# Performance work log

Measured on AMD Instinct MI355X. Metric: run time of the kernel, lower is better.

The kernel has to match this reference:

```python
import jax, jax.numpy as jnp
import numpy as np

FS = 11        # filter_size
N_ITER = 5     # mean-field iterations


def _unfold(x, fs):
    """x: (B, C, Hp, Wp) padded -> patches (B, C, H, W, fs, fs) with
    patches[b,c,h,w,i,j] == x[b,c,h+i,w+j]."""
    B, C, Hp, Wp = x.shape
    H, W = Hp - fs + 1, Wp - fs + 1
    p = jax.lax.conv_general_dilated_patches(
        x.reshape(B * C, 1, Hp, Wp), (fs, fs), (1, 1), 'VALID')  # (B*C, fs*fs, H, W)
    return p.reshape(B, C, fs, fs, H, W).transpose(0, 1, 4, 5, 2, 3)


def _smoothing_filter(fs, inv_bw, spacings):
    """Gaussian spatial filter with zeroed center, shape (B, fs, fs)."""
    r = jnp.arange(-(fs // 2), fs // 2 + 1, dtype=spacings.dtype)
    d = jnp.stack(jnp.meshgrid(r, r, indexing='ij'))           # (2, fs, fs)
    d = d[None] * spacings[:, :, None, None]                   # (B, 2, fs, fs)
    f = jnp.exp(-jnp.sum((d * inv_bw) ** 2 / 2, axis=1))       # (B, fs, fs)
    return f.at[:, fs // 2, fs // 2].set(0.0)


def setup_inputs() -> dict:
    key = jax.random.key(0)
    k1, k2 = jax.random.split(key)
    B, C, CH, H, W = 2, 6, 3, 192, 192
    return {
        'x': jax.random.normal(k1, (B, C, H, W), dtype=jnp.float32),
        'features': jax.random.normal(k2, (B, CH, H, W), dtype=jnp.float32),
        'spatial_spacings': jnp.ones((B, 2), dtype=jnp.float32),
        'smoothing_weight': jnp.array(1.0, dtype=jnp.float32),
        'appearance_weight': jnp.array(1.0, dtype=jnp.float32),
        'inverse_smoothing_bandwidth': jnp.array(1.0, dtype=jnp.float32),
        'inverse_appearance_bandwidth': jnp.array(1.0, dtype=jnp.float32),
    }


def reference(x, features, spatial_spacings, smoothing_weight, appearance_weight,
              inverse_smoothing_bandwidth, inverse_appearance_bandwidth):
    fs, pad = FS, FS // 2
    B, C, H, W = x.shape
    pad_cfg = [(0, 0), (0, 0), (pad, pad), (pad, pad)]

    # Spatial Gaussian filter (iteration-independent).
    sf = _smoothing_filter(fs, inverse_smoothing_bandwidth, spatial_spacings)  # (B,fs,fs)

    # Bilateral (appearance) filter, also iteration-independent -> hoisted.
    fpatch = _unfold(jnp.pad(features, pad_cfg), fs)           # (B,ch,H,W,fs,fs)
    diffs = features[..., None, None] - fpatch
    af = jnp.exp(-jnp.sum((diffs * inverse_appearance_bandwidth) ** 2 / 2, axis=1))  # (B,H,W,fs,fs)
    af = af.at[..., fs // 2, fs // 2].set(0.0)

    # combined message filter: w_s * sf + w_a * sf * af  (center tap already zero)
    sfb = sf[:, None, None]                                    # (B,1,1,fs,fs)
    total_filter = smoothing_weight * jnp.broadcast_to(sfb, af.shape) + appearance_weight * sfb * af

    compat = -jnp.eye(C, dtype=x.dtype)                        # Potts compatibility mu(l,l') = -[l==l']
    negative_unary = x
    for _ in range(N_ITER):
        q = jax.nn.softmax(x, axis=1)
        qpatch = _unfold(jnp.pad(q, pad_cfg), fs)              # (B,C,H,W,fs,fs)
        msg = jnp.einsum('bhwij,bchwij->bchw', total_filter, qpatch)
        x = negative_unary - jnp.einsum('bjhw,jk->bkhw', msg, compat)
    return jax.nn.log_softmax(x, axis=1)
```

## Files before the change

kernel.cpp:

```cpp
#include <hip/hip_runtime.h>

#define HH 192
#define WW 192
#define BB 2
#define NC 6
#define FSZ 11
#define PAD 5
#define TW 16
#define TH 8
#define SWD 26
#define SHT 18
#define LA 33
#define HW (HH*WW)
#define BT 512

__device__ __forceinline__ unsigned pkbf(float a, float b) {
    unsigned ua = (__float_as_uint(a) + 0x8000u) >> 16;
    unsigned ub = (__float_as_uint(b) + 0x8000u) & 0xffff0000u;
    return ua | ub;
}
__device__ __forceinline__ float lo16(unsigned u){ return __uint_as_float(u << 16); }
__device__ __forceinline__ float hi16(unsigned u){ return __uint_as_float(u & 0xffff0000u); }

template<bool FIRST, bool LAST>
__global__ __launch_bounds__(BT, 4)
void crf_iter(const float* __restrict__ xpl, const uint4* __restrict__ Ain,
              const float* __restrict__ f2in, const float* __restrict__ feats,
              const float* __restrict__ spac, const float* __restrict__ swp,
              const float* __restrict__ awp, const float* __restrict__ isbp,
              const float* __restrict__ iabp,
              uint4* __restrict__ Aout, float* __restrict__ f2out,
              float* __restrict__ outp)
{
    __shared__ uint4 A[SHT][LA];
    __shared__ float F2[SHT][LA];
    __shared__ float sfw[FSZ*FSZ];
    __shared__ float sfa[FSZ*FSZ];
    __shared__ float pm[8][NC][132];

    const int tid = threadIdx.x;
    const int b  = blockIdx.z;
    const int w0 = blockIdx.x * TW;
    const int h0 = blockIdx.y * TH;

    const float swv = swp[0], awv = awp[0], isb = isbp[0], iab = iabp[0];
    const float s0 = spac[b*2], s1 = spac[b*2+1];
    const float sfac = iab * 0.70710678f;

    if (tid < FSZ*FSZ) {
        const int fi = tid / FSZ, fj = tid - (tid/FSZ)*FSZ;
        const float ri = (float)(fi-PAD) * s0 * isb;
        const float rj = (float)(fj-PAD) * s1 * isb;
        float sf = __expf(-0.5f*(ri*ri + rj*rj));
        if (fi == PAD && fj == PAD) sf = 0.f;
        sfw[tid] = sf * swv;
        sfa[tid] = sf * awv;
    }

    for (int idx = tid; idx < SHT*SWD; idx += BT) {
        const int sr = idx / SWD, sc = idx - (idx/SWD)*SWD;
        const int gh = h0 + sr - PAD, gw = w0 + sc - PAD;
        uint4 av = make_uint4(0u,0u,0u,0u);
        float f2v = 0.f;
        if (gh >= 0 && gh < HH && gw >= 0 && gw < WW) {
            if (FIRST) {
                const int off = gh*WW + gw;
                const float* xb = xpl + (size_t)b*NC*HW + off;
                const float v0 = xb[0];
                const float v1 = xb[HW];
                const float v2 = xb[2*HW];
                const float v3 = xb[3*HW];
                const float v4 = xb[4*HW];
                const float v5 = xb[5*HW];
                float m = fmaxf(fmaxf(fmaxf(v0,v1),fmaxf(v2,v3)),fmaxf(v4,v5));
                float q0=__expf(v0-m), q1=__expf(v1-m), q2=__expf(v2-m);
                float q3=__expf(v3-m), q4=__expf(v4-m), q5=__expf(v5-m);
                const float rs = 1.0f/(q0+q1+q2+q3+q4+q5);
                q0*=rs; q1*=rs; q2*=rs; q3*=rs; q4*=rs; q5*=rs;
                const float* fb = feats + (size_t)b*3*HW + off;
                const float g0 = fb[0]*sfac, g1 = fb[HW]*sfac, g2 = fb[2*HW]*sfac;
                av = make_uint4(pkbf(q0,q1), pkbf(q2,q3), pkbf(q4,q5), pkbf(g0,g1));
                f2v = g2;
            } else {
                const size_t p = (size_t)(b*HH + gh)*WW + gw;
                av  = Ain[p];
                f2v = f2in[p];
            }
        }
        A[sr][sc]  = av;
        F2[sr][sc] = f2v;
    }

    const int w    = tid >> 6;
    const int l    = tid & 63;
    const int half = l >> 5;
    const int lh   = l & 31;
    const int ry   = lh >> 2;
    const int lc0  = (lh & 3) * 4;
    const int jb   = half * 6;

    __syncthreads();

    float cf0[4], cf1[4], cf2[4];
    #pragma unroll
    for (int k = 0; k < 4; ++k) {
        const unsigned fw = A[ry+PAD][lc0+PAD+k].w;
        cf0[k] = lo16(fw);
        cf1[k] = hi16(fw);
        cf2[k] = F2[ry+PAD][lc0+PAD+k];
    }

    float msg[4][NC];
    #pragma unroll
    for (int k = 0; k < 4; ++k)
        #pragma unroll
        for (int c = 0; c < NC; ++c) msg[k][c] = 0.f;

    auto row_pass = [&](int i) {
        const int r = ry + i;
        const uint4* Ar = &A[r][lc0 + jb];
        const float* Fr = &F2[r][lc0 + jb];
        float srwR[6], sraR[6];
        #pragma unroll
        for (int d = 0; d < 6; ++d) {
            const int jj = jb + d;
            const bool v = (jj < FSZ);
            srwR[d] = v ? sfw[i*FSZ + jj] : 0.f;
            sraR[d] = v ? sfa[i*FSZ + jj] : 0.f;
        }
        #pragma unroll
        for (int a = 0; a < 8; ++a) {
            const uint4 av = Ar[a];
            const float g2 = Fr[a];
            const float q0 = lo16(av.x), q1 = hi16(av.x);
            const float q2 = lo16(av.y), q3 = hi16(av.y);
            const float q4 = lo16(av.z), q5 = hi16(av.z);
            const float g0 = lo16(av.w), g1 = hi16(av.w);
            #pragma unroll
            for (int k = 0; k < 4; ++k) {
                const int d = a - k;
                if (d < 0 || d > 5) continue;
                const float d0 = cf0[k]-g0, d1 = cf1[k]-g1, d2 = cf2[k]-g2;
                const float t  = fmaf(d2,d2, fmaf(d1,d1, d0*d0));
                const float af = __expf(-t);
                const float tf = fmaf(af, sraR[d], srwR[d]);
                msg[k][0] = fmaf(tf,q0,msg[k][0]);
                msg[k][1] = fmaf(tf,q1,msg[k][1]);
                msg[k][2] = fmaf(tf,q2,msg[k][2]);
                msg[k][3] = fmaf(tf,q3,msg[k][3]);
                msg[k][4] = fmaf(tf,q4,msg[k][4]);
                msg[k][5] = fmaf(tf,q5,msg[k][5]);
            }
        }
        if (jb == 0) {
            const uint4 av = Ar[8];
            const float g2 = Fr[8];
            const float q0 = lo16(av.x), q1 = hi16(av.x);
            const float q2 = lo16(av.y), q3 = hi16(av.y);
            const float q4 = lo16(av.z), q5 = hi16(av.z);
            const float g0 = lo16(av.w), g1 = hi16(av.w);
            const float d0 = cf0[3]-g0, d1 = cf1[3]-g1, d2 = cf2[3]-g2;
            const float t  = fmaf(d2,d2, fmaf(d1,d1, d0*d0));
            const float af = __expf(-t);
            const float tf = fmaf(af, sraR[5], srwR[5]);
            msg[3][0] = fmaf(tf,q0,msg[3][0]);
            msg[3][1] = fmaf(tf,q1,msg[3][1]);
            msg[3][2] = fmaf(tf,q2,msg[3][2]);
            msg[3][3] = fmaf(tf,q3,msg[3][3]);
            msg[3][4] = fmaf(tf,q4,msg[3][4]);
            msg[3][5] = fmaf(tf,q5,msg[3][5]);
        }
    };

    row_pass(w);
    if (w < 3) row_pass(w + 8);

    #pragma unroll
    for (int k = 0; k < 4; ++k)
        #pragma unroll
        for (int c = 0; c < NC; ++c)
            msg[k][c] += __shfl_xor(msg[k][c], 32);

    if (half == 0) {
        #pragma unroll
        for (int c = 0; c < NC; ++c) {
            float4 v = make_float4(msg[0][c], msg[1][c], msg[2][c], msg[3][c]);
            *(float4*)&pm[w][c][ry*16 + lc0] = v;
        }
    }
    __syncthreads();

    if (tid < TW*TH) {
        const int col = tid & 15, rw = tid >> 4;
        float xn[NC];
        #pragma unroll
        for (int c = 0; c < NC; ++c) {
            float s = 0.f;
            #pragma unroll
            for (int g = 0; g < 8; ++g) s += pm[g][c][tid];
            xn[c] = s;
        }
        const int gh = h0 + rw, gw = w0 + col;
        const size_t pb = (size_t)b*NC*HW + (size_t)gh*WW + gw;
        #pragma unroll
        for (int c = 0; c < NC; ++c) xn[c] += xpl[pb + (size_t)c*HW];

        float m = xn[0];
        #pragma unroll
        for (int c = 1; c < NC; ++c) m = fmaxf(m, xn[c]);

        if (LAST) {
            float s = 0.f;
            #pragma unroll
            for (int c = 0; c < NC; ++c) s += __expf(xn[c]-m);
            const float lg = m + __logf(s);
            #pragma unroll
            for (int c = 0; c < NC; ++c) outp[pb + (size_t)c*HW] = xn[c] - lg;
        } else {
            float e[NC]; float s = 0.f;
            #pragma unroll
            for (int c = 0; c < NC; ++c) { e[c] = __expf(xn[c]-m); s += e[c]; }
            const float rs = 1.0f / s;
            const unsigned f01 = A[rw+PAD][col+PAD].w;
            const size_t p = (size_t)(b*HH + gh)*WW + gw;
            Aout[p] = make_uint4(pkbf(e[0]*rs, e[1]*rs),
                                 pkbf(e[2]*rs, e[3]*rs),
                                 pkbf(e[4]*rs, e[5]*rs), f01);
            if (FIRST) f2out[p] = F2[rw+PAD][col+PAD];
        }
    }
}

extern "C" void kernel_launch(void* const* d_in, const int* in_sizes, int n_in,
                              void* d_out, int out_size, void* d_ws, size_t ws_size,
                              hipStream_t stream)
{
    const float* x    = (const float*)d_in[0];
    const float* fts  = (const float*)d_in[1];
    const float* spc  = (const float*)d_in[2];
    const float* swp  = (const float*)d_in[3];
    const float* awp  = (const float*)d_in[4];
    const float* isbp = (const float*)d_in[5];
    const float* iabp = (const float*)d_in[6];
    float* out = (float*)d_out;

    uint4* A0  = (uint4*)d_ws;
    uint4* A1  = A0 + (size_t)BB*HW;
    float* f2s = (float*)(A1 + (size_t)BB*HW);

    dim3 grid(WW/TW, HH/TH, BB);
    dim3 blk(BT);

    crf_iter<true ,false><<<grid, blk, 0, stream>>>(x, A1, f2s, fts, spc, swp, awp, isbp, iabp, A0, f2s, out);
    crf_iter<false,false><<<grid, blk, 0, stream>>>(x, A0, f2s, fts, spc, swp, awp, isbp, iabp, A1, f2s, out);
    crf_iter<false,false><<<grid, blk, 0, stream>>>(x, A1, f2s, fts, spc, swp, awp, isbp, iabp, A0, f2s, out);
    crf_iter<false,false><<<grid, blk, 0, stream>>>(x, A0, f2s, fts, spc, swp, awp, isbp, iabp, A1, f2s, out);
    crf_iter<false,true ><<<grid, blk, 0, stream>>>(x, A1, f2s, fts, spc, swp, awp, isbp, iabp, A0, f2s, out);
}
```

Measured before the change: 64.34 us.

## Fuse two mean-field iterations per kernel using halo recomputation

Each launch now runs two CRF iterations. The first iteration is computed over an expanded tile that includes the filter halo, and its softmax result is kept in shared memory as the input to the second iteration. The final iteration runs in a separate kernel that applies log-softmax, so the launch count drops from five to three and the intermediate global round-trips are reduced. In exchange, the first stage of each pair recomputes messages for the whole halo region, which greatly increases exp and FMA work per output pixel. Thread utilisation also changes: 234 of 512 lanes-pairs are used in the first stage, and the second stage uses a 4-way row split.

```diff
diff --git a/kernel.cpp b/kernel.cpp
--- a/kernel.cpp
+++ b/kernel.cpp
@@ -8,11 +8,15 @@
 #define PAD 5
 #define TW 16
 #define TH 8
-#define SWD 26
-#define SHT 18
-#define LA 33
+#define SW2 36
+#define SH2 28
+#define LA1 37
+#define MW 26
+#define MH 18
+#define LA2 27
 #define HW (HH*WW)
 #define BT 512
+#define NPAIR 234
 
 __device__ __forceinline__ unsigned pkbf(float a, float b) {
     unsigned ua = (__float_as_uint(a) + 0x8000u) >> 16;
@@ -22,31 +26,9 @@
 __device__ __forceinline__ float lo16(unsigned u){ return __uint_as_float(u << 16); }
 __device__ __forceinline__ float hi16(unsigned u){ return __uint_as_float(u & 0xffff0000u); }
 
-template<bool FIRST, bool LAST>
-__global__ __launch_bounds__(BT, 4)
-void crf_iter(const float* __restrict__ xpl, const uint4* __restrict__ Ain,
-              const float* __restrict__ f2in, const float* __restrict__ feats,
-              const float* __restrict__ spac, const float* __restrict__ swp,
-              const float* __restrict__ awp, const float* __restrict__ isbp,
-              const float* __restrict__ iabp,
-              uint4* __restrict__ Aout, float* __restrict__ f2out,
-              float* __restrict__ outp)
+__device__ __forceinline__ void build_sf(int tid, float s0, float s1, float isb,
+                                         float swv, float awv, float* sfw, float* sfa)
 {
-    __shared__ uint4 A[SHT][LA];
-    __shared__ float F2[SHT][LA];
-    __shared__ float sfw[FSZ*FSZ];
-    __shared__ float sfa[FSZ*FSZ];
-    __shared__ float pm[8][NC][132];
-
-    const int tid = threadIdx.x;
-    const int b  = blockIdx.z;
-    const int w0 = blockIdx.x * TW;
-    const int h0 = blockIdx.y * TH;
-
-    const float swv = swp[0], awv = awp[0], isb = isbp[0], iab = iabp[0];
-    const float s0 = spac[b*2], s1 = spac[b*2+1];
-    const float sfac = iab * 0.70710678f;
-
     if (tid < FSZ*FSZ) {
         const int fi = tid / FSZ, fj = tid - (tid/FSZ)*FSZ;
         const float ri = (float)(fi-PAD) * s0 * isb;
@@ -56,30 +38,53 @@
         sfw[tid] = sf * swv;
         sfa[tid] = sf * awv;
     }
-
-    for (int idx = tid; idx < SHT*SWD; idx += BT) {
-        const int sr = idx / SWD, sc = idx - (idx/SWD)*SWD;
-        const int gh = h0 + sr - PAD, gw = w0 + sc - PAD;
+}
+
+template<bool FIRST>
+__global__ __launch_bounds__(BT, 4)
+void crf_pair(const float* __restrict__ xpl, const uint4* __restrict__ Ain,
+              const float* __restrict__ f2in, const float* __restrict__ feats,
+              const float* __restrict__ spac, const float* __restrict__ swp,
+              const float* __restrict__ awp, const float* __restrict__ isbp,
+              const float* __restrict__ iabp,
+              uint4* __restrict__ Aout, float* __restrict__ f2out)
+{
+    __shared__ uint4 A1[SH2][LA1];
+    __shared__ float F2a[SH2][LA1];
+    __shared__ uint4 Q1[MH][LA2];
+    __shared__ float sfw[FSZ*FSZ], sfa[FSZ*FSZ];
+    __shared__ float pm[4][NC][132];
+
+    const int tid = threadIdx.x;
+    const int b  = blockIdx.z;
+    const int w0 = blockIdx.x * TW;
+    const int h0 = blockIdx.y * TH;
+
+    const float swv = swp[0], awv = awp[0], isb = isbp[0], iab = iabp[0];
+    const float s0 = spac[b*2], s1 = spac[b*2+1];
+    const float sfac = iab * 0.70710678f;
+
+    build_sf(tid, s0, s1, isb, swv, awv, sfw, sfa);
+
+    for (int idx = tid; idx < SH2*LA1; idx += BT) {
+        const int sr = idx / LA1, sc = idx - (idx/LA1)*LA1;
+        const int gh = h0 - 2*PAD + sr, gw = w0 - 2*PAD + sc;
         uint4 av = make_uint4(0u,0u,0u,0u);
         float f2v = 0.f;
         if (gh >= 0 && gh < HH && gw >= 0 && gw < WW) {
             if (FIRST) {
                 const int off = gh*WW + gw;
                 const float* xb = xpl + (size_t)b*NC*HW + off;
-                const float v0 = xb[0];
-                const float v1 = xb[HW];
-                const float v2 = xb[2*HW];
-                const float v3 = xb[3*HW];
-                const float v4 = xb[4*HW];
-                const float v5 = xb[5*HW];
+                const float v0 = xb[0], v1 = xb[HW], v2 = xb[2*HW];
+                const float v3 = xb[3*HW], v4 = xb[4*HW], v5 = xb[5*HW];
                 float m = fmaxf(fmaxf(fmaxf(v0,v1),fmaxf(v2,v3)),fmaxf(v4,v5));
                 float q0=__expf(v0-m), q1=__expf(v1-m), q2=__expf(v2-m);
                 float q3=__expf(v3-m), q4=__expf(v4-m), q5=__expf(v5-m);
                 const float rs = 1.0f/(q0+q1+q2+q3+q4+q5);
-                q0*=rs; q1*=rs; q2*=rs; q3*=rs; q4*=rs; q5*=rs;
                 const float* fb = feats + (size_t)b*3*HW + off;
                 const float g0 = fb[0]*sfac, g1 = fb[HW]*sfac, g2 = fb[2*HW]*sfac;
-                av = make_uint4(pkbf(q0,q1), pkbf(q2,q3), pkbf(q4,q5), pkbf(g0,g1));
+                av = make_uint4(pkbf(q0*rs,q1*rs), pkbf(q2*rs,q3*rs),
+                                pkbf(q4*rs,q5*rs), pkbf(g0,g1));
                 f2v = g2;
             } else {
                 const size_t p = (size_t)(b*HH + gh)*WW + gw;
@@ -87,147 +92,264 @@
                 f2v = f2in[p];
             }
         }
-        A[sr][sc]  = av;
-        F2[sr][sc] = f2v;
-    }
-
-    const int w    = tid >> 6;
-    const int l    = tid & 63;
-    const int half = l >> 5;
-    const int lh   = l & 31;
-    const int ry   = lh >> 2;
-    const int lc0  = (lh & 3) * 4;
-    const int jb   = half * 6;
-
-    __syncthreads();
-
-    float cf0[4], cf1[4], cf2[4];
-    #pragma unroll
-    for (int k = 0; k < 4; ++k) {
-        const unsigned fw = A[ry+PAD][lc0+PAD+k].w;
-        cf0[k] = lo16(fw);
-        cf1[k] = hi16(fw);
-        cf2[k] = F2[ry+PAD][lc0+PAD+k];
-    }
-
-    float msg[4][NC];
-    #pragma unroll
-    for (int k = 0; k < 4; ++k)
-        #pragma unroll
-        for (int c = 0; c < NC; ++c) msg[k][c] = 0.f;
-
-    auto row_pass = [&](int i) {
-        const int r = ry + i;
-        const uint4* Ar = &A[r][lc0 + jb];
-        const float* Fr = &F2[r][lc0 + jb];
-        float srwR[6], sraR[6];
-        #pragma unroll
-        for (int d = 0; d < 6; ++d) {
-            const int jj = jb + d;
-            const bool v = (jj < FSZ);
-            srwR[d] = v ? sfw[i*FSZ + jj] : 0.f;
-            sraR[d] = v ? sfa[i*FSZ + jj] : 0.f;
-        }
-        #pragma unroll
-        for (int a = 0; a < 8; ++a) {
-            const uint4 av = Ar[a];
-            const float g2 = Fr[a];
-            const float q0 = lo16(av.x), q1 = hi16(av.x);
-            const float q2 = lo16(av.y), q3 = hi16(av.y);
-            const float q4 = lo16(av.z), q5 = hi16(av.z);
-            const float g0 = lo16(av.w), g1 = hi16(av.w);
+        A1[sr][sc]  = av;
+        F2a[sr][sc] = f2v;
+    }
+    __syncthreads();
+
+    {
+        const int half = tid & 1;
+        const int pr   = tid >> 1;
+        if (pr < NPAIR) {
+            const int r1 = pr / 13;
+            const int c0 = (pr - r1*13) * 2;
+            const int jb = half * 6;
+
+            const unsigned cwA = A1[r1+PAD][c0+PAD].w;
+            const unsigned cwB = A1[r1+PAD][c0+PAD+1].w;
+            const float a0 = lo16(cwA), a1 = hi16(cwA), a2 = F2a[r1+PAD][c0+PAD];
+            const float b0 = lo16(cwB), b1 = hi16(cwB), b2 = F2a[r1+PAD][c0+PAD+1];
+
+            float mA[NC], mB[NC];
             #pragma unroll
-            for (int k = 0; k < 4; ++k) {
-                const int d = a - k;
-                if (d < 0 || d > 5) continue;
-                const float d0 = cf0[k]-g0, d1 = cf1[k]-g1, d2 = cf2[k]-g2;
-                const float t  = fmaf(d2,d2, fmaf(d1,d1, d0*d0));
-                const float af = __expf(-t);
-                const float tf = fmaf(af, sraR[d], srwR[d]);
-                msg[k][0] = fmaf(tf,q0,msg[k][0]);
-                msg[k][1] = fmaf(tf,q1,msg[k][1]);
-                msg[k][2] = fmaf(tf,q2,msg[k][2]);
-                msg[k][3] = fmaf(tf,q3,msg[k][3]);
-                msg[k][4] = fmaf(tf,q4,msg[k][4]);
-                msg[k][5] = fmaf(tf,q5,msg[k][5]);
-            }
-        }
-        if (jb == 0) {
-            const uint4 av = Ar[8];
-            const float g2 = Fr[8];
-            const float q0 = lo16(av.x), q1 = hi16(av.x);
-            const float q2 = lo16(av.y), q3 = hi16(av.y);
-            const float q4 = lo16(av.z), q5 = hi16(av.z);
-            const float g0 = lo16(av.w), g1 = hi16(av.w);
-            const float d0 = cf0[3]-g0, d1 = cf1[3]-g1, d2 = cf2[3]-g2;
-            const float t  = fmaf(d2,d2, fmaf(d1,d1, d0*d0));
-            const float af = __expf(-t);
-            const float tf = fmaf(af, sraR[5], srwR[5]);
-            msg[3][0] = fmaf(tf,q0,msg[3][0]);
-            msg[3][1] = fmaf(tf,q1,msg[3][1]);
-            msg[3][2] = fmaf(tf,q2,msg[3][2]);
-            msg[3][3] = fmaf(tf,q3,msg[3][3]);
-            msg[3][4] = fmaf(tf,q4,msg[3][4]);
-            msg[3][5] = fmaf(tf,q5,msg[3][5]);
-        }
-    };
-
-    row_pass(w);
-    if (w < 3) row_pass(w + 8);
-
-    #pragma unroll
-    for (int k = 0; k < 4; ++k)
+            for (int c = 0; c < NC; ++c) { mA[c]=0.f; mB[c]=0.f; }
+
+            #pragma unroll 1
+            for (int i = 0; i < FSZ; ++i) {
+                float srwR[6], sraR[6];
+                #pragma unroll
+                for (int d = 0; d < 6; ++d) {
+                    const int jj = jb + d;
+                    const bool v = (jj < FSZ);
+                    srwR[d] = v ? sfw[i*FSZ + jj] : 0.f;
+                    sraR[d] = v ? sfa[i*FSZ + jj] : 0.f;
+                }
+                const uint4* Ar = &A1[r1+i][c0+jb];
+                const float* Fr = &F2a[r1+i][c0+jb];
+                #pragma unroll
+                for (int a = 0; a < 7; ++a) {
+                    const uint4 av = Ar[a];
+                    const float g2 = Fr[a];
+                    const float q0 = lo16(av.x), q1 = hi16(av.x);
+                    const float q2 = lo16(av.y), q3 = hi16(av.y);
+                    const float q4 = lo16(av.z), q5 = hi16(av.z);
+                    const float g0 = lo16(av.w), g1 = hi16(av.w);
+                    if (a < 6) {
+                        const float d0=a0-g0, d1=a1-g1, d2=a2-g2;
+                        const float tt = fmaf(d2,d2, fmaf(d1,d1, d0*d0));
+                        const float af = __expf(-tt);
+                        const float tf = fmaf(af, sraR[a], srwR[a]);
+                        mA[0]=fmaf(tf,q0,mA[0]); mA[1]=fmaf(tf,q1,mA[1]);
+                        mA[2]=fmaf(tf,q2,mA[2]); mA[3]=fmaf(tf,q3,mA[3]);
+                        mA[4]=fmaf(tf,q4,mA[4]); mA[5]=fmaf(tf,q5,mA[5]);
+                    }
+                    if (a >= 1) {
+                        const float d0=b0-g0, d1=b1-g1, d2=b2-g2;
+                        const float tt = fmaf(d2,d2, fmaf(d1,d1, d0*d0));
+                        const float af = __expf(-tt);
+                        const float tf = fmaf(af, sraR[a-1], srwR[a-1]);
+                        mB[0]=fmaf(tf,q0,mB[0]); mB[1]=fmaf(tf,q1,mB[1]);
+                        mB[2]=fmaf(tf,q2,mB[2]); mB[3]=fmaf(tf,q3,mB[3]);
+                        mB[4]=fmaf(tf,q4,mB[4]); mB[5]=fmaf(tf,q5,mB[5]);
+                    }
+                }
+            }
+
+            #pragma unroll
+            for (int c = 0; c < NC; ++c) {
+                mA[c] += __shfl_xor(mA[c], 1);
+                mB[c] += __shfl_xor(mB[c], 1);
+            }
+
+            if (half == 0) {
+                const int gh = h0 - PAD + r1;
+                #pragma unroll
+                for (int k = 0; k < 2; ++k) {
+                    const int gw = w0 - PAD + c0 + k;
+                    const float* msg = k ? mB : mA;
+                    uint4 qv = make_uint4(0u,0u,0u,0u);
+                    if (gh >= 0 && gh < HH && gw >= 0 && gw < WW) {
+                        const float* up = xpl + (size_t)b*NC*HW + (size_t)gh*WW + gw;
+                        float xn[NC];
+                        #pragma unroll
+                        for (int c = 0; c < NC; ++c) xn[c] = up[(size_t)c*HW] + msg[c];
+                        float m = xn[0];
+                        #pragma unroll
+                        for (int c = 1; c < NC; ++c) m = fmaxf(m, xn[c]);
+                        float e[NC], s = 0.f;
+                        #pragma unroll
+                        for (int c = 0; c < NC; ++c) { e[c] = __expf(xn[c]-m); s += e[c]; }
+                        const float rs = 1.0f / s;
+                        qv = make_uint4(pkbf(e[0]*rs,e[1]*rs), pkbf(e[2]*rs,e[3]*rs),
+                                        pkbf(e[4]*rs,e[5]*rs), k ? cwB : cwA);
+                    }
+                    Q1[r1][c0+k] = qv;
+                }
+            }
+        }
+    }
+    __syncthreads();
+
+    {
+        const int g = tid >> 7, p = tid & 127;
+        const int pr = p >> 4, pc = p & 15;
+        const unsigned cw = A1[pr+2*PAD][pc+2*PAD].w;
+        const float c0f = lo16(cw), c1f = hi16(cw), c2f = F2a[pr+2*PAD][pc+2*PAD];
+        float m2[NC];
+        #pragma unroll
+        for (int c = 0; c < NC; ++c) m2[c] = 0.f;
+
+        #pragma unroll 1
+        for (int ii = 0; ii < 3; ++ii) {
+            const int i = g + 4*ii;
+            if (i < FSZ) {
+                const float* srw = &sfw[i*FSZ];
+                const float* sra = &sfa[i*FSZ];
+                const uint4* Qr = &Q1[pr+i][pc];
+                const float* Fr = &F2a[pr+i+PAD][pc+PAD];
+                #pragma unroll
+                for (int j = 0; j < FSZ; ++j) {
+                    const uint4 av = Qr[j];
+                    const float g2 = Fr[j];
+                    const float q0 = lo16(av.x), q1 = hi16(av.x);
+                    const float q2 = lo16(av.y), q3 = hi16(av.y);
+                    const float q4 = lo16(av.z), q5 = hi16(av.z);
+                    const float g0 = lo16(av.w), g1 = hi16(av.w);
+                    const float d0=c0f-g0, d1=c1f-g1, d2=c2f-g2;
+                    const float tt = fmaf(d2,d2, fmaf(d1,d1, d0*d0));
+                    const float af = __expf(-tt);
+                    const float tf = fmaf(af, sra[j], srw[j]);
+                    m2[0]=fmaf(tf,q0,m2[0]); m2[1]=fmaf(tf,q1,m2[1]);
+                    m2[2]=fmaf(tf,q2,m2[2]); m2[3]=fmaf(tf,q3,m2[3]);
+                    m2[4]=fmaf(tf,q4,m2[4]); m2[5]=fmaf(tf,q5,m2[5]);
+                }
+            }
+        }
+        #pragma unroll
+        for (int c = 0; c < NC; ++c) pm[g][c][p] = m2[c];
+    }
+    __syncthreads();
+
+    if (tid < 128) {
+        const int pr = tid >> 4, pc = tid & 15;
+        float xn[NC];
         #pragma unroll
         for (int c = 0; c < NC; ++c)
-            msg[k][c] += __shfl_xor(msg[k][c], 32);
-
-    if (half == 0) {
-        #pragma unroll
-        for (int c = 0; c < NC; ++c) {
-            float4 v = make_float4(msg[0][c], msg[1][c], msg[2][c], msg[3][c]);
-            *(float4*)&pm[w][c][ry*16 + lc0] = v;
-        }
-    }
-    __syncthreads();
-
-    if (tid < TW*TH) {
-        const int col = tid & 15, rw = tid >> 4;
+            xn[c] = pm[0][c][tid] + pm[1][c][tid] + pm[2][c][tid] + pm[3][c][tid];
+        const int gh = h0 + pr, gw = w0 + pc;
+        const float* up = xpl + (size_t)b*NC*HW + (size_t)gh*WW + gw;
+        #pragma unroll
+        for (int c = 0; c < NC; ++c) xn[c] += up[(size_t)c*HW];
+        float m = xn[0];
+        #pragma unroll
+        for (int c = 1; c < NC; ++c) m = fmaxf(m, xn[c]);
+        float e[NC], s = 0.f;
+        #pragma unroll
+        for (int c = 0; c < NC; ++c) { e[c] = __expf(xn[c]-m); s += e[c]; }
+        const float rs = 1.0f / s;
+        const size_t p = (size_t)(b*HH + gh)*WW + gw;
+        Aout[p] = make_uint4(pkbf(e[0]*rs,e[1]*rs), pkbf(e[2]*rs,e[3]*rs),
+                             pkbf(e[4]*rs,e[5]*rs), A1[pr+2*PAD][pc+2*PAD].w);
+        if (FIRST) f2out[p] = F2a[pr+2*PAD][pc+2*PAD];
+    }
+}
+
+__global__ __launch_bounds__(BT, 4)
+void crf_last(const float* __restrict__ xpl, const uint4* __restrict__ Ain,
+              const float* __restrict__ f2in,
+              const float* __restrict__ spac, const float* __restrict__ swp,
+              const float* __restrict__ awp, const float* __restrict__ isbp,
+              const float* __restrict__ iabp, float* __restrict__ outp)
+{
+    __shared__ uint4 Ac[MH][LA2];
+    __shared__ float F2c[MH][LA2];
+    __shared__ float sfw[FSZ*FSZ], sfa[FSZ*FSZ];
+    __shared__ float pm[4][NC][132];
+
+    const int tid = threadIdx.x;
+    const int b  = blockIdx.z;
+    const int w0 = blockIdx.x * TW;
+    const int h0 = blockIdx.y * TH;
+
+    const float swv = swp[0], awv = awp[0], isb = isbp[0];
+    const float s0 = spac[b*2], s1 = spac[b*2+1];
+
+    build_sf(tid, s0, s1, isb, swv, awv, sfw, sfa);
+
+    for (int idx = tid; idx < MH*MW; idx += BT) {
+        const int sr = idx / MW, sc = idx - (idx/MW)*MW;
+        const int gh = h0 - PAD + sr, gw = w0 - PAD + sc;
+        uint4 av = make_uint4(0u,0u,0u,0u);
+        float f2v = 0.f;
+        if (gh >= 0 && gh < HH && gw >= 0 && gw < WW) {
+            const size_t p = (size_t)(b*HH + gh)*WW + gw;
+            av  = Ain[p];
+            f2v = f2in[p];
+        }
+        Ac[sr][sc]  = av;
+        F2c[sr][sc] = f2v;
+    }
+    __syncthreads();
+
+    {
+        const int g = tid >> 7, p = tid & 127;
+        const int pr = p >> 4, pc = p & 15;
+        const unsigned cw = Ac[pr+PAD][pc+PAD].w;
+        const float c0f = lo16(cw), c1f = hi16(cw), c2f = F2c[pr+PAD][pc+PAD];
+        float m2[NC];
+        #pragma unroll
+        for (int c = 0; c < NC; ++c) m2[c] = 0.f;
+
+        #pragma unroll 1
+        for (int ii = 0; ii < 3; ++ii) {
+            const int i = g + 4*ii;
+            if (i < FSZ) {
+                const float* srw = &sfw[i*FSZ];
+                const float* sra = &sfa[i*FSZ];
+                const uint4* Qr = &Ac[pr+i][pc];
+                const float* Fr = &F2c[pr+i][pc];
+                #pragma unroll
+                for (int j = 0; j < FSZ; ++j) {
+                    const uint4 av = Qr[j];
+                    const float g2 = Fr[j];
+                    const float q0 = lo16(av.x), q1 = hi16(av.x);
+                    const float q2 = lo16(av.y), q3 = hi16(av.y);
+                    const float q4 = lo16(av.z), q5 = hi16(av.z);
+                    const float g0 = lo16(av.w), g1 = hi16(av.w);
+                    const float d0=c0f-g0, d1=c1f-g1, d2=c2f-g2;
+                    const float tt = fmaf(d2,d2, fmaf(d1,d1, d0*d0));
+                    const float af = __expf(-tt);
+                    const float tf = fmaf(af, sra[j], srw[j]);
+                    m2[0]=fmaf(tf,q0,m2[0]); m2[1]=fmaf(tf,q1,m2[1]);
+                    m2[2]=fmaf(tf,q2,m2[2]); m2[3]=fmaf(tf,q3,m2[3]);
+                    m2[4]=fmaf(tf,q4,m2[4]); m2[5]=fmaf(tf,q5,m2[5]);
+                }
+            }
+        }
+        #pragma unroll
+        for (int c = 0; c < NC; ++c) pm[g][c][p] = m2[c];
+    }
+    __syncthreads();
+
+    if (tid < 128) {
+        const int pr = tid >> 4, pc = tid & 15;
         float xn[NC];
         #pragma unroll
-        for (int c = 0; c < NC; ++c) {
-            float s = 0.f;
-            #pragma unroll
-            for (int g = 0; g < 8; ++g) s += pm[g][c][tid];
-            xn[c] = s;
-        }
-        const int gh = h0 + rw, gw = w0 + col;
+        for (int c = 0; c < NC; ++c)
+            xn[c] = pm[0][c][tid] + pm[1][c][tid] + pm[2][c][tid] + pm[3][c][tid];
+        const int gh = h0 + pr, gw = w0 + pc;
         const size_t pb = (size_t)b*NC*HW + (size_t)gh*WW + gw;
         #pragma unroll
         for (int c = 0; c < NC; ++c) xn[c] += xpl[pb + (size_t)c*HW];
-
         float m = xn[0];
         #pragma unroll
         for (int c = 1; c < NC; ++c) m = fmaxf(m, xn[c]);
-
-        if (LAST) {
-            float s = 0.f;
-            #pragma unroll
-            for (int c = 0; c < NC; ++c) s += __expf(xn[c]-m);
-            const float lg = m + __logf(s);
-            #pragma unroll
-            for (int c = 0; c < NC; ++c) outp[pb + (size_t)c*HW] = xn[c] - lg;
-        } else {
-            float e[NC]; float s = 0.f;
-            #pragma unroll
-            for (int c = 0; c < NC; ++c) { e[c] = __expf(xn[c]-m); s += e[c]; }
-            const float rs = 1.0f / s;
-            const unsigned f01 = A[rw+PAD][col+PAD].w;
-            const size_t p = (size_t)(b*HH + gh)*WW + gw;
-            Aout[p] = make_uint4(pkbf(e[0]*rs, e[1]*rs),
-                                 pkbf(e[2]*rs, e[3]*rs),
-                                 pkbf(e[4]*rs, e[5]*rs), f01);
-            if (FIRST) f2out[p] = F2[rw+PAD][col+PAD];
-        }
+        float s = 0.f;
+        #pragma unroll
+        for (int c = 0; c < NC; ++c) s += __expf(xn[c]-m);
+        const float lg = m + __logf(s);
+        #pragma unroll
+        for (int c = 0; c < NC; ++c) outp[pb + (size_t)c*HW] = xn[c] - lg;
     }
 }
 
@@ -251,9 +373,7 @@
     dim3 grid(WW/TW, HH/TH, BB);
     dim3 blk(BT);
 
-    crf_iter<true ,false><<<grid, blk, 0, stream>>>(x, A1, f2s, fts, spc, swp, awp, isbp, iabp, A0, f2s, out);
-    crf_iter<false,false><<<grid, blk, 0, stream>>>(x, A0, f2s, fts, spc, swp, awp, isbp, iabp, A1, f2s, out);
-    crf_iter<false,false><<<grid, blk, 0, stream>>>(x, A1, f2s, fts, spc, swp, awp, isbp, iabp, A0, f2s, out);
-    crf_iter<false,false><<<grid, blk, 0, stream>>>(x, A0, f2s, fts, spc, swp, awp, isbp, iabp, A1, f2s, out);
-    crf_iter<false,true ><<<grid, blk, 0, stream>>>(x, A1, f2s, fts, spc, swp, awp, isbp, iabp, A0, f2s, out);
-}
+    crf_pair<true ><<<grid, blk, 0, stream>>>(x, A0, f2s, fts, spc, swp, awp, isbp, iabp, A0, f2s);
+    crf_pair<false><<<grid, blk, 0, stream>>>(x, A0, f2s, fts, spc, swp, awp, isbp, iabp, A1, f2s);
+    crf_last<<<grid, blk, 0, stream>>>(x, A1, f2s, spc, swp, awp, isbp, iabp, out);
+}
```

New measurement: 97.32 us. +51.3%, slower.

## Precompute bilateral filter weights once and stream them in each iteration

Applied to the files above, without the earlier changes.

Adds a separate kernel that computes the full 121-tap combined spatial/appearance filter per pixel into workspace, stored in fp32. Each mean-field iteration then reads these precomputed weights from global memory instead of recomputing exp() on feature differences. This removes the transcendental work that was repeated five times, at the cost of about 36 MB of filter traffic per iteration (2x121x192x192 floats). Thread mapping is also simplified to one pixel per thread, with 256 threads per block and two row halves.

```diff
diff --git a/kernel.cpp b/kernel.cpp
--- a/kernel.cpp
+++ b/kernel.cpp
@@ -6,13 +6,14 @@
 #define NC 6
 #define FSZ 11
 #define PAD 5
+#define NT (FSZ*FSZ)
 #define TW 16
 #define TH 8
 #define SWD 26
 #define SHT 18
-#define LA 33
+#define LA 27
 #define HW (HH*WW)
-#define BT 512
+#define BT 256
 
 __device__ __forceinline__ unsigned pkbf(float a, float b) {
     unsigned ua = (__float_as_uint(a) + 0x8000u) >> 16;
@@ -22,21 +23,15 @@
 __device__ __forceinline__ float lo16(unsigned u){ return __uint_as_float(u << 16); }
 __device__ __forceinline__ float hi16(unsigned u){ return __uint_as_float(u & 0xffff0000u); }
 
-template<bool FIRST, bool LAST>
-__global__ __launch_bounds__(BT, 4)
-void crf_iter(const float* __restrict__ xpl, const uint4* __restrict__ Ain,
-              const float* __restrict__ f2in, const float* __restrict__ feats,
-              const float* __restrict__ spac, const float* __restrict__ swp,
-              const float* __restrict__ awp, const float* __restrict__ isbp,
-              const float* __restrict__ iabp,
-              uint4* __restrict__ Aout, float* __restrict__ f2out,
-              float* __restrict__ outp)
+__global__ __launch_bounds__(BT)
+void crf_filt(const float* __restrict__ feats, const float* __restrict__ spac,
+              const float* __restrict__ swp, const float* __restrict__ awp,
+              const float* __restrict__ isbp, const float* __restrict__ iabp,
+              float* __restrict__ filt)
 {
-    __shared__ uint4 A[SHT][LA];
-    __shared__ float F2[SHT][LA];
-    __shared__ float sfw[FSZ*FSZ];
-    __shared__ float sfa[FSZ*FSZ];
-    __shared__ float pm[8][NC][132];
+    __shared__ float2 F01[SHT][LA];
+    __shared__ float  F2s[SHT][LA];
+    __shared__ float  sfw[NT], sfa[NT];
 
     const int tid = threadIdx.x;
     const int b  = blockIdx.z;
@@ -45,9 +40,9 @@
 
     const float swv = swp[0], awv = awp[0], isb = isbp[0], iab = iabp[0];
     const float s0 = spac[b*2], s1 = spac[b*2+1];
-    const float sfac = iab * 0.70710678f;
-
-    if (tid < FSZ*FSZ) {
+    const float kapp = -0.5f * iab * iab;
+
+    if (tid < NT) {
         const int fi = tid / FSZ, fj = tid - (tid/FSZ)*FSZ;
         const float ri = (float)(fi-PAD) * s0 * isb;
         const float rj = (float)(fj-PAD) * s1 * isb;
@@ -57,153 +52,127 @@
         sfa[tid] = sf * awv;
     }
 
+    const float* fb = feats + (size_t)b*3*HW;
+    for (int idx = tid; idx < SHT*SWD; idx += BT) {
+        const int sr = idx / SWD, sc = idx - (idx/SWD)*SWD;
+        const int gh = h0 + sr - PAD, gw = w0 + sc - PAD;
+        float g0=0.f, g1=0.f, g2=0.f;
+        if (gh >= 0 && gh < HH && gw >= 0 && gw < WW) {
+            const int off = gh*WW + gw;
+            g0 = fb[off]; g1 = fb[off+HW]; g2 = fb[off+2*HW];
+        }
+        F01[sr][sc] = make_float2(g0,g1);
+        F2s[sr][sc] = g2;
+    }
+    __syncthreads();
+
+    const int g2g = tid >> 7;
+    const int p   = tid & 127;
+    const int ry  = p >> 4;
+    const int tx  = p & 15;
+    const int gh  = h0 + ry, gw = w0 + tx;
+
+    const float2 c01 = F01[ry+PAD][tx+PAD];
+    const float  c2  = F2s[ry+PAD][tx+PAD];
+
+    float* fo = filt + (size_t)b*NT*HW + (size_t)gh*WW + gw;
+
+    const int i0 = g2g ? 6 : 0;
+    const int i1 = g2g ? FSZ : 6;
+    #pragma unroll 1
+    for (int i = i0; i < i1; ++i) {
+        #pragma unroll
+        for (int j = 0; j < FSZ; ++j) {
+            const int t = i*FSZ + j;
+            const float2 g01 = F01[ry+i][tx+j];
+            const float  g2v = F2s[ry+i][tx+j];
+            const float d0 = c01.x-g01.x, d1 = c01.y-g01.y, d2 = c2-g2v;
+            const float tt = fmaf(d2,d2, fmaf(d1,d1, d0*d0));
+            const float af = __expf(tt * kapp);
+            fo[(size_t)t*HW] = fmaf(af, sfa[t], sfw[t]);
+        }
+    }
+}
+
+template<bool FIRST, bool LAST>
+__global__ __launch_bounds__(BT)
+void crf_it(const float* __restrict__ xpl, const uint4* __restrict__ Ain,
+            const float* __restrict__ filt,
+            uint4* __restrict__ Aout, float* __restrict__ outp)
+{
+    __shared__ uint4 As[SHT][LA];
+    __shared__ float pm[2][NC][128];
+
+    const int tid = threadIdx.x;
+    const int b  = blockIdx.z;
+    const int w0 = blockIdx.x * TW;
+    const int h0 = blockIdx.y * TH;
+
     for (int idx = tid; idx < SHT*SWD; idx += BT) {
         const int sr = idx / SWD, sc = idx - (idx/SWD)*SWD;
         const int gh = h0 + sr - PAD, gw = w0 + sc - PAD;
         uint4 av = make_uint4(0u,0u,0u,0u);
-        float f2v = 0.f;
         if (gh >= 0 && gh < HH && gw >= 0 && gw < WW) {
             if (FIRST) {
-                const int off = gh*WW + gw;
-                const float* xb = xpl + (size_t)b*NC*HW + off;
-                const float v0 = xb[0];
-                const float v1 = xb[HW];
-                const float v2 = xb[2*HW];
-                const float v3 = xb[3*HW];
-                const float v4 = xb[4*HW];
-                const float v5 = xb[5*HW];
+                const float* xb = xpl + (size_t)b*NC*HW + gh*WW + gw;
+                const float v0 = xb[0], v1 = xb[HW], v2 = xb[2*HW];
+                const float v3 = xb[3*HW], v4 = xb[4*HW], v5 = xb[5*HW];
                 float m = fmaxf(fmaxf(fmaxf(v0,v1),fmaxf(v2,v3)),fmaxf(v4,v5));
                 float q0=__expf(v0-m), q1=__expf(v1-m), q2=__expf(v2-m);
                 float q3=__expf(v3-m), q4=__expf(v4-m), q5=__expf(v5-m);
                 const float rs = 1.0f/(q0+q1+q2+q3+q4+q5);
-                q0*=rs; q1*=rs; q2*=rs; q3*=rs; q4*=rs; q5*=rs;
-                const float* fb = feats + (size_t)b*3*HW + off;
-                const float g0 = fb[0]*sfac, g1 = fb[HW]*sfac, g2 = fb[2*HW]*sfac;
-                av = make_uint4(pkbf(q0,q1), pkbf(q2,q3), pkbf(q4,q5), pkbf(g0,g1));
-                f2v = g2;
+                av = make_uint4(pkbf(q0*rs,q1*rs), pkbf(q2*rs,q3*rs),
+                                pkbf(q4*rs,q5*rs), 0u);
             } else {
-                const size_t p = (size_t)(b*HH + gh)*WW + gw;
-                av  = Ain[p];
-                f2v = f2in[p];
+                av = Ain[(size_t)(b*HH + gh)*WW + gw];
             }
         }
-        A[sr][sc]  = av;
-        F2[sr][sc] = f2v;
-    }
-
-    const int w    = tid >> 6;
-    const int l    = tid & 63;
-    const int half = l >> 5;
-    const int lh   = l & 31;
-    const int ry   = lh >> 2;
-    const int lc0  = (lh & 3) * 4;
-    const int jb   = half * 6;
-
+        As[sr][sc] = av;
+    }
     __syncthreads();
 
-    float cf0[4], cf1[4], cf2[4];
+    const int g2g = tid >> 7;
+    const int p   = tid & 127;
+    const int ry  = p >> 4;
+    const int tx  = p & 15;
+    const int gh  = h0 + ry, gw = w0 + tx;
+
+    const float* fbase = filt + (size_t)b*NT*HW + (size_t)gh*WW + gw;
+
+    float msg[NC];
     #pragma unroll
-    for (int k = 0; k < 4; ++k) {
-        const unsigned fw = A[ry+PAD][lc0+PAD+k].w;
-        cf0[k] = lo16(fw);
-        cf1[k] = hi16(fw);
-        cf2[k] = F2[ry+PAD][lc0+PAD+k];
-    }
-
-    float msg[4][NC];
+    for (int c = 0; c < NC; ++c) msg[c] = 0.f;
+
+    const int i0 = g2g ? 6 : 0;
+    const int i1 = g2g ? FSZ : 6;
+    #pragma unroll 2
+    for (int i = i0; i < i1; ++i) {
+        const int r = ry + i;
+        #pragma unroll
+        for (int j = 0; j < FSZ; ++j) {
+            const uint4 av = As[r][tx+j];
+            const float tf = fbase[(size_t)(i*FSZ + j)*HW];
+            msg[0] = fmaf(tf, lo16(av.x), msg[0]);
+            msg[1] = fmaf(tf, hi16(av.x), msg[1]);
+            msg[2] = fmaf(tf, lo16(av.y), msg[2]);
+            msg[3] = fmaf(tf, hi16(av.y), msg[3]);
+            msg[4] = fmaf(tf, lo16(av.z), msg[4]);
+            msg[5] = fmaf(tf, hi16(av.z), msg[5]);
+        }
+    }
+
     #pragma unroll
-    for (int k = 0; k < 4; ++k)
-        #pragma unroll
-        for (int c = 0; c < NC; ++c) msg[k][c] = 0.f;
-
-    auto row_pass = [&](int i) {
-        const int r = ry + i;
-        const uint4* Ar = &A[r][lc0 + jb];
-        const float* Fr = &F2[r][lc0 + jb];
-        float srwR[6], sraR[6];
-        #pragma unroll
-        for (int d = 0; d < 6; ++d) {
-            const int jj = jb + d;
-            const bool v = (jj < FSZ);
-            srwR[d] = v ? sfw[i*FSZ + jj] : 0.f;
-            sraR[d] = v ? sfa[i*FSZ + jj] : 0.f;
-        }
-        #pragma unroll
-        for (int a = 0; a < 8; ++a) {
-            const uint4 av = Ar[a];
-            const float g2 = Fr[a];
-            const float q0 = lo16(av.x), q1 = hi16(av.x);
-            const float q2 = lo16(av.y), q3 = hi16(av.y);
-            const float q4 = lo16(av.z), q5 = hi16(av.z);
-            const float g0 = lo16(av.w), g1 = hi16(av.w);
-            #pragma unroll
-            for (int k = 0; k < 4; ++k) {
-                const int d = a - k;
-                if (d < 0 || d > 5) continue;
-                const float d0 = cf0[k]-g0, d1 = cf1[k]-g1, d2 = cf2[k]-g2;
-                const float t  = fmaf(d2,d2, fmaf(d1,d1, d0*d0));
-                const float af = __expf(-t);
-                const float tf = fmaf(af, sraR[d], srwR[d]);
-                msg[k][0] = fmaf(tf,q0,msg[k][0]);
-                msg[k][1] = fmaf(tf,q1,msg[k][1]);
-                msg[k][2] = fmaf(tf,q2,msg[k][2]);
-                msg[k][3] = fmaf(tf,q3,msg[k][3]);
-                msg[k][4] = fmaf(tf,q4,msg[k][4]);
-                msg[k][5] = fmaf(tf,q5,msg[k][5]);
-            }
-        }
-        if (jb == 0) {
-            const uint4 av = Ar[8];
-            const float g2 = Fr[8];
-            const float q0 = lo16(av.x), q1 = hi16(av.x);
-            const float q2 = lo16(av.y), q3 = hi16(av.y);
-            const float q4 = lo16(av.z), q5 = hi16(av.z);
-            const float g0 = lo16(av.w), g1 = hi16(av.w);
-            const float d0 = cf0[3]-g0, d1 = cf1[3]-g1, d2 = cf2[3]-g2;
-            const float t  = fmaf(d2,d2, fmaf(d1,d1, d0*d0));
-            const float af = __expf(-t);
-            const float tf = fmaf(af, sraR[5], srwR[5]);
-            msg[3][0] = fmaf(tf,q0,msg[3][0]);
-            msg[3][1] = fmaf(tf,q1,msg[3][1]);
-            msg[3][2] = fmaf(tf,q2,msg[3][2]);
-            msg[3][3] = fmaf(tf,q3,msg[3][3]);
-            msg[3][4] = fmaf(tf,q4,msg[3][4]);
-            msg[3][5] = fmaf(tf,q5,msg[3][5]);
-        }
-    };
-
-    row_pass(w);
-    if (w < 3) row_pass(w + 8);
-
-    #pragma unroll
-    for (int k = 0; k < 4; ++k)
+    for (int c = 0; c < NC; ++c) pm[g2g][c][p] = msg[c];
+    __syncthreads();
+
+    if (tid < 128) {
+        const int pr = tid >> 4, pc = tid & 15;
+        const int oh = h0 + pr, ow = w0 + pc;
+        const size_t pb = (size_t)b*NC*HW + (size_t)oh*WW + ow;
+        float xn[NC];
         #pragma unroll
         for (int c = 0; c < NC; ++c)
-            msg[k][c] += __shfl_xor(msg[k][c], 32);
-
-    if (half == 0) {
-        #pragma unroll
-        for (int c = 0; c < NC; ++c) {
-            float4 v = make_float4(msg[0][c], msg[1][c], msg[2][c], msg[3][c]);
-            *(float4*)&pm[w][c][ry*16 + lc0] = v;
-        }
-    }
-    __syncthreads();
-
-    if (tid < TW*TH) {
-        const int col = tid & 15, rw = tid >> 4;
-        float xn[NC];
-        #pragma unroll
-        for (int c = 0; c < NC; ++c) {
-            float s = 0.f;
-            #pragma unroll
-            for (int g = 0; g < 8; ++g) s += pm[g][c][tid];
-            xn[c] = s;
-        }
-        const int gh = h0 + rw, gw = w0 + col;
-        const size_t pb = (size_t)b*NC*HW + (size_t)gh*WW + gw;
-        #pragma unroll
-        for (int c = 0; c < NC; ++c) xn[c] += xpl[pb + (size_t)c*HW];
+            xn[c] = pm[0][c][tid] + pm[1][c][tid] + xpl[pb + (size_t)c*HW];
 
         float m = xn[0];
         #pragma unroll
@@ -217,16 +186,13 @@
             #pragma unroll
             for (int c = 0; c < NC; ++c) outp[pb + (size_t)c*HW] = xn[c] - lg;
         } else {
-            float e[NC]; float s = 0.f;
+            float e[NC], s = 0.f;
             #pragma unroll
             for (int c = 0; c < NC; ++c) { e[c] = __expf(xn[c]-m); s += e[c]; }
             const float rs = 1.0f / s;
-            const unsigned f01 = A[rw+PAD][col+PAD].w;
-            const size_t p = (size_t)(b*HH + gh)*WW + gw;
-            Aout[p] = make_uint4(pkbf(e[0]*rs, e[1]*rs),
-                                 pkbf(e[2]*rs, e[3]*rs),
-                                 pkbf(e[4]*rs, e[5]*rs), f01);
-            if (FIRST) f2out[p] = F2[rw+PAD][col+PAD];
+            Aout[(size_t)(b*HH + oh)*WW + ow] =
+                make_uint4(pkbf(e[0]*rs,e[1]*rs), pkbf(e[2]*rs,e[3]*rs),
+                           pkbf(e[4]*rs,e[5]*rs), 0u);
         }
     }
 }
@@ -244,16 +210,17 @@
     const float* iabp = (const float*)d_in[6];
     float* out = (float*)d_out;
 
-    uint4* A0  = (uint4*)d_ws;
-    uint4* A1  = A0 + (size_t)BB*HW;
-    float* f2s = (float*)(A1 + (size_t)BB*HW);
+    float* filt = (float*)d_ws;
+    uint4* A0   = (uint4*)((char*)d_ws + (size_t)BB*NT*HW*sizeof(float));
+    uint4* A1   = A0 + (size_t)BB*HW;
 
     dim3 grid(WW/TW, HH/TH, BB);
     dim3 blk(BT);
 
-    crf_iter<true ,false><<<grid, blk, 0, stream>>>(x, A1, f2s, fts, spc, swp, awp, isbp, iabp, A0, f2s, out);
-    crf_iter<false,false><<<grid, blk, 0, stream>>>(x, A0, f2s, fts, spc, swp, awp, isbp, iabp, A1, f2s, out);
-    crf_iter<false,false><<<grid, blk, 0, stream>>>(x, A1, f2s, fts, spc, swp, awp, isbp, iabp, A0, f2s, out);
-    crf_iter<false,false><<<grid, blk, 0, stream>>>(x, A0, f2s, fts, spc, swp, awp, isbp, iabp, A1, f2s, out);
-    crf_iter<false,true ><<<grid, blk, 0, stream>>>(x, A1, f2s, fts, spc, swp, awp, isbp, iabp, A0, f2s, out);
-}
+    crf_filt<<<grid, blk, 0, stream>>>(fts, spc, swp, awp, isbp, iabp, filt);
+    crf_it<true ,false><<<grid, blk, 0, stream>>>(x, A1, filt, A0, out);
+    crf_it<false,false><<<grid, blk, 0, stream>>>(x, A0, filt, A1, out);
+    crf_it<false,false><<<grid, blk, 0, stream>>>(x, A1, filt, A0, out);
+    crf_it<false,false><<<grid, blk, 0, stream>>>(x, A0, filt, A1, out);
+    crf_it<false,true ><<<grid, blk, 0, stream>>>(x, A1, filt, A0, out);
+}
```

After: 89.70 us. 1.39x slower.
